# Kernel tuning notes

Hardware: AMD Instinct MI355X
Metric: run time of the kernel (lower is better)

Reference implementation:

```python
import jax, jax.numpy as jnp
import numpy as np

DIM = 512; D_STATE = 8; D_CONV = 3; EXPAND = 1; WIN = 7; N = WIN * WIN
D_INNER = EXPAND * DIM; D_HALF = D_INNER // 2
DT_RANK = -(-DIM // 16)  # 32
E = DT_RANK + 2 * D_STATE  # 48
B_WIN = 512


def _diag_flat(w):
    idx = []
    for s in range(2 * w - 1):
        for r in range(max(0, s - (w - 1)), min(w - 1, s) + 1):
            idx.append(r * w + (s - r))
    return np.array(idx, dtype=np.int32)


def _anti_flat(w):
    idx = []
    for s in range(2 * w - 1):
        for r in range(max(0, s - (w - 1)), min(w - 1, s) + 1):
            c = s - r
            idx.append(r * w + (w - 1 - c))
    return np.array(idx, dtype=np.int32)

DIAG_IDX = jnp.asarray(_diag_flat(WIN))
ANTI_IDX = jnp.asarray(_anti_flat(WIN))
V_IDX = jnp.asarray(np.arange(N).reshape(WIN, WIN).T.reshape(-1).astype(np.int32))


def setup_inputs() -> dict:
    key = jax.random.key(0)
    ks = iter(jax.random.split(key, 32))
    f32 = jnp.float32
    def lin_w(k, out_d, in_d):
        return (jax.random.normal(k, (out_d, in_d), f32) * (in_d ** -0.5)).astype(f32)
    inp = {}
    inp['tokens'] = jax.random.normal(next(ks), (B_WIN, N, DIM), f32)
    for nm in ['pre_h', 'pre_v', 'pre_d', 'pre_a', 'post_h', 'post_v', 'post_d', 'post_a']:
        inp[nm + '_w'] = lin_w(next(ks), DIM, DIM)
        inp[nm + '_b'] = jnp.zeros((DIM,), f32)
    inp['in_proj_w'] = lin_w(next(ks), D_INNER, DIM)
    inp['conv_x_w'] = jax.random.normal(next(ks), (D_HALF, 1, D_CONV), f32) * (D_CONV ** -0.5)
    inp['conv_x_b'] = jnp.zeros((D_HALF,), f32)
    inp['conv_z_w'] = jax.random.normal(next(ks), (D_HALF, 1, D_CONV), f32) * (D_CONV ** -0.5)
    inp['conv_z_b'] = jnp.zeros((D_HALF,), f32)
    inp['x_proj_w'] = lin_w(next(ks), E, D_HALF)
    inp['ln_w'] = jnp.ones((E,), f32)
    inp['ln_b'] = jnp.zeros((E,), f32)
    dt_std = DT_RANK ** -0.5
    inp['dt_proj_w'] = jax.random.uniform(next(ks), (D_HALF, DT_RANK), f32, -dt_std, dt_std)
    u = jax.random.uniform(next(ks), (D_HALF,), f32)
    dt = jnp.clip(jnp.exp(u * (np.log(0.1) - np.log(0.001)) + np.log(0.001)), 1e-4, None)
    inp['dt_proj_b'] = dt + jnp.log(-jnp.expm1(-dt))
    inp['A_log'] = jnp.tile(jnp.log(jnp.arange(1, D_STATE + 1, dtype=f32))[None, :], (D_HALF, 1))
    inp['D_param'] = jnp.ones((D_HALF,), f32)
    inp['out_proj_w'] = lin_w(next(ks), DIM, D_INNER)
    inp['gate_logits'] = jnp.zeros((4,), f32)
    return inp


def _linear(x, W, b=None):
    y = x @ W.T
    return y if b is None else y + b


def _dwconv_same(x, w, b):
    # x: (b, d, l), w: (d, 1, k) depthwise, cross-correlation like torch
    y = jax.lax.conv_general_dilated(x, w, window_strides=(1,), padding='SAME',
                                     dimension_numbers=('NCH', 'OIH', 'NCH'),
                                     feature_group_count=x.shape[1])
    return y + b[None, :, None]


def _layernorm(x, g, b, eps=1e-5):
    m = jnp.mean(x, -1, keepdims=True)
    v = jnp.var(x, -1, keepdims=True)
    return (x - m) * jax.lax.rsqrt(v + eps) * g + b


def _selective_scan(u, delta, A, Bm, Cm, D, delta_bias):
    # u, delta: (b,d,l); A: (d,n); Bm, Cm: (b,n,l); D: (d,)
    delta = jax.nn.softplus(delta + delta_bias[None, :, None])
    u_l = jnp.moveaxis(u, 2, 0)       # (l,b,d)
    d_l = jnp.moveaxis(delta, 2, 0)   # (l,b,d)
    B_l = jnp.moveaxis(Bm, 2, 0)      # (l,b,n)
    C_l = jnp.moveaxis(Cm, 2, 0)      # (l,b,n)
    h0 = jnp.zeros((u.shape[0], u.shape[1], A.shape[1]), u.dtype)  # (b,d,n)

    def step(h, t):
        dt_t, u_t, B_t, C_t = t
        dA = jnp.exp(dt_t[:, :, None] * A[None])          # (b,d,n)
        dBu = dt_t[:, :, None] * B_t[:, None, :] * u_t[:, :, None]
        h = h * dA + dBu
        y = jnp.einsum('bdn,bn->bd', h, C_t)
        return h, y

    _, ys = jax.lax.scan(step, h0, (d_l, u_l, B_l, C_l))
    y = jnp.moveaxis(ys, 0, 2)  # (b,d,l)
    return y + D[None, :, None] * u


def _mamba_core(x_seq, p):
    b, L, _ = x_seq.shape
    xz = _linear(x_seq, p['in_proj_w'])              # (b,l,d_inner)
    xz = jnp.swapaxes(xz, 1, 2)                      # (b,d_inner,l)
    x, z = jnp.split(xz, 2, axis=1)                  # each (b,d_half,l)
    x_conv = jax.nn.silu(_dwconv_same(x, p['conv_x_w'], p['conv_x_b']))
    z_conv = jax.nn.silu(_dwconv_same(z, p['conv_z_w'], p['conv_z_b']))
    A = -jnp.exp(p['A_log'])
    x_dbl = jnp.einsum('bdl,ed->ble', x_conv, p['x_proj_w'])  # (b,l,E)
    x_dbl = _layernorm(x_dbl, p['ln_w'], p['ln_b'])
    dt, Bm, Cm = jnp.split(x_dbl, [DT_RANK, DT_RANK + D_STATE], axis=-1)
    dt = jnp.swapaxes(_linear(dt, p['dt_proj_w']), 1, 2)      # (b,d_half,l)
    Bm = jnp.swapaxes(Bm, 1, 2)                                # (b,n,l)
    Cm = jnp.swapaxes(Cm, 1, 2)
    y = _selective_scan(x_conv, dt, A, Bm, Cm, p['D_param'], p['dt_proj_b'])
    y = jnp.nan_to_num(y)
    y = jnp.concatenate([y, z_conv], axis=1)                   # (b,d_inner,l)
    y = jnp.swapaxes(y, 1, 2)
    return _linear(y, p['out_proj_w'])


def reference(tokens, pre_h_w, pre_h_b, pre_v_w, pre_v_b, pre_d_w, pre_d_b,
              pre_a_w, pre_a_b, in_proj_w, conv_x_w, conv_x_b, conv_z_w, conv_z_b,
              x_proj_w, ln_w, ln_b, dt_proj_w, dt_proj_b, A_log, D_param,
              out_proj_w, post_h_w, post_h_b, post_v_w, post_v_b, post_d_w,
              post_d_b, post_a_w, post_a_b, gate_logits):
    p = dict(in_proj_w=in_proj_w, conv_x_w=conv_x_w, conv_x_b=conv_x_b,
             conv_z_w=conv_z_w, conv_z_b=conv_z_b, x_proj_w=x_proj_w,
             ln_w=ln_w, ln_b=ln_b, dt_proj_w=dt_proj_w, dt_proj_b=dt_proj_b,
             A_log=A_log, D_param=D_param, out_proj_w=out_proj_w)
    rh = _linear(tokens, pre_h_w, pre_h_b)
    rv = _linear(tokens, pre_v_w, pre_v_b)[:, V_IDX, :]
    rd = _linear(tokens, pre_d_w, pre_d_b)[:, DIAG_IDX, :]
    ra = _linear(tokens, pre_a_w, pre_a_b)[:, ANTI_IDX, :]
    r_all = jnp.concatenate([rh, rv, rd, ra], axis=0)
    y_all = _mamba_core(r_all, p)
    yh, yv, yd, ya = jnp.split(y_all, 4, axis=0)
    yh = _linear(yh, post_h_w, post_h_b)
    yv = _linear(yv, post_v_w, post_v_b)
    yd = _linear(yd, post_d_w, post_d_b)
    ya = _linear(ya, post_a_w, post_a_b)
    g = jax.nn.softmax(gate_logits)
    return g[0] * yh + g[1] * yv + g[2] * yd + g[3] * ya
```

## Files before the change

### kernel.cpp

```cpp
#include <hip/hip_runtime.h>
#include <stdint.h>

typedef __attribute__((ext_vector_type(8))) short bf16x8;
typedef __attribute__((ext_vector_type(4))) float f32x4;

__device__ __forceinline__ float bf2f(short u){
  union { float f; uint32_t i; } v; v.i = ((uint32_t)(uint16_t)u) << 16; return v.f;
}
__device__ __forceinline__ short f2bf(float x){
  union { float f; uint32_t i; } v; v.f = x;
  uint32_t r = v.i + 0x7FFFu + ((v.i >> 16) & 1u);
  return (short)(r >> 16);
}

__device__ __forceinline__ void gl_lds16(const short* g, short* l){
  __builtin_amdgcn_global_load_lds(
      (__attribute__((address_space(1))) void*)(short*)g,
      (__attribute__((address_space(3))) void*)l, 16, 0, 0);
}

__device__ const int d_DIAG[49] = {0,1,7,2,8,14,3,9,15,21,4,10,16,22,28,5,11,17,23,29,35,
  6,12,18,24,30,36,42,13,19,25,31,37,43,20,26,32,38,44,27,33,39,45,34,40,46,41,47,48};
__device__ const int d_ANTI[49] = {6,5,13,4,12,20,3,11,19,27,2,10,18,26,34,1,9,17,25,33,41,
  0,8,16,24,32,40,48,7,15,23,31,39,47,14,22,30,38,46,21,29,37,45,28,36,44,35,43,42};

__device__ __forceinline__ int perm_idx(int g, int l){
  if (g == 0) return l;
  if (g == 1) return (l % 7) * 7 + l / 7;
  if (g == 2) return d_DIAG[l];
  return d_ANTI[l];
}

template<int NT>
__device__ __forceinline__ void kcore256(
    const short* aU0, const short* aU1, const short* bU0, const short* bU1,
    short* S, int w, int lane, f32x4 acc[8][4])
{
  int wr = w >> 2, wc = w & 3;
  int mr = lane & 15, quad = lane >> 4;
  int sw = (quad ^ ((mr >> 1) & 3)) * 8;
  auto STAGE = [&](int u, int t){
    short* base = S + (t & 1) * 16384;
    if      (u == 0) gl_lds16(aU0 + t*32, base + (w*32)*32);
    else if (u == 1) gl_lds16(aU1 + t*32, base + (w*32 + 16)*32);
    else if (u == 2) gl_lds16(bU0 + t*32, base + 8192 + (w*32)*32);
    else             gl_lds16(bU1 + t*32, base + 8192 + (w*32 + 16)*32);
  };
  STAGE(0,0); STAGE(1,0); STAGE(2,0); STAGE(3,0);
  if (NT > 1){ STAGE(0,1); STAGE(1,1); }
  asm volatile("s_waitcnt vmcnt(2)" ::: "memory");
  __builtin_amdgcn_s_barrier();
  for (int t = 0; t < NT; ++t){
    const short* Ab = S + (t & 1) * 16384;
    const short* Bb = Ab + 8192;
    bf16x8 bfr[4];
    #pragma unroll
    for (int nf = 0; nf < 4; ++nf)
      bfr[nf] = *(const bf16x8*)(Bb + (wc*64 + nf*16 + mr)*32 + sw);
    #pragma unroll
    for (int ph = 0; ph < 4; ++ph){
      bf16x8 af[2];
      #pragma unroll
      for (int mi = 0; mi < 2; ++mi)
        af[mi] = *(const bf16x8*)(Ab + (wr*128 + (ph*2+mi)*16 + mr)*32 + sw);
      if (ph < 2 && t+1 < NT) STAGE(2+ph, t+1);
      #pragma unroll
      for (int mi = 0; mi < 2; ++mi)
        #pragma unroll
        for (int nf = 0; nf < 4; ++nf)
          acc[ph*2+mi][nf] = __builtin_amdgcn_mfma_f32_16x16x32_bf16(af[mi], bfr[nf], acc[ph*2+mi][nf],0,0,0);
    }
    __builtin_amdgcn_s_barrier();
    if (t+2 < NT){
      STAGE(0, t+2); STAGE(1, t+2);
      asm volatile("s_waitcnt vmcnt(2)" ::: "memory");
    } else if (t+1 < NT){
      asm volatile("s_waitcnt vmcnt(0)" ::: "memory");
    }
    __builtin_amdgcn_s_barrier();
  }
}

template<int NT>
__device__ __forceinline__ void kcore256x128(
    const short* aU0, const short* aU1, const short* bU,
    short* S, int w, int lane, f32x4 acc[4][4])
{
  int wr = w >> 1, wc = w & 1;
  int mr = lane & 15, quad = lane >> 4;
  int sw = (quad ^ ((mr >> 1) & 3)) * 8;
  auto STAGE_A = [&](int t){
    short* base = S + (t & 1) * 12288;
    gl_lds16(aU0 + t*32, base + (w*32)*32);
    gl_lds16(aU1 + t*32, base + (w*32 + 16)*32);
  };
  auto STAGE_B = [&](int t){
    short* base = S + (t & 1) * 12288;
    gl_lds16(bU + t*32, base + 8192 + (w*16)*32);
  };
  STAGE_A(0); STAGE_B(0);
  if (NT > 1) STAGE_A(1);
  asm volatile("s_waitcnt vmcnt(2)" ::: "memory");
  __builtin_amdgcn_s_barrier();
  for (int t = 0; t < NT; ++t){
    const short* Ab = S + (t & 1) * 12288;
    const short* Bb = Ab + 8192;
    bf16x8 bfr[4];
    #pragma unroll
    for (int nf = 0; nf < 4; ++nf)
      bfr[nf] = *(const bf16x8*)(Bb + (wc*64 + nf*16 + mr)*32 + sw);
    #pragma unroll
    for (int ph = 0; ph < 4; ++ph){
      bf16x8 af = *(const bf16x8*)(Ab + (wr*64 + ph*16 + mr)*32 + sw);
      if (ph == 1 && t+1 < NT) STAGE_B(t+1);
      #pragma unroll
      for (int nf = 0; nf < 4; ++nf)
        acc[ph][nf] = __builtin_amdgcn_mfma_f32_16x16x32_bf16(af, bfr[nf], acc[ph][nf],0,0,0);
    }
    __builtin_amdgcn_s_barrier();
    if (t+2 < NT){
      STAGE_A(t+2);
      asm volatile("s_waitcnt vmcnt(2)" ::: "memory");
    } else if (t+1 < NT){
      asm volatile("s_waitcnt vmcnt(0)" ::: "memory");
    }
    __builtin_amdgcn_s_barrier();
  }
}

__global__ __launch_bounds__(256) void k_conv_all(
    const float* __restrict__ in_proj,
    const float* __restrict__ pw0, const float* __restrict__ pw1,
    const float* __restrict__ pw2, const float* __restrict__ pw3,
    const float* __restrict__ xpw, const float* __restrict__ dtw,
    short* __restrict__ inp_bf, short* __restrict__ postw_bf,
    short* __restrict__ xpw_bf, short* __restrict__ dtw_bf)
{
  int q = blockIdx.x*256 + threadIdx.x;
  const float* src; short* dst; int off;
  if (q < 65536){ src = in_proj; dst = inp_bf; off = q; }
  else if (q < 65536 + 262144){
    int r = q - 65536; int g = r >> 16; int loc = r & 65535;
    src = (g==0)?pw0:(g==1)?pw1:(g==2)?pw2:pw3;
    dst = postw_bf + g*262144; off = loc;
  }
  else if (q < 65536 + 262144 + 3072){ src = xpw; dst = xpw_bf; off = q - (65536+262144); }
  else { src = dtw; dst = dtw_bf; off = q - (65536+262144+3072); }
  float4 v = *(const float4*)(src + off*4);
  uint32_t p0 = (uint32_t)(uint16_t)f2bf(v.x) | ((uint32_t)(uint16_t)f2bf(v.y) << 16);
  uint32_t p1 = (uint32_t)(uint16_t)f2bf(v.z) | ((uint32_t)(uint16_t)f2bf(v.w) << 16);
  uint2 p; p.x = p0; p.y = p1;
  *(uint2*)(dst + off*4) = p;
}

__global__ __launch_bounds__(256) void k_transp(
    const float* __restrict__ pw0, const float* __restrict__ pw1,
    const float* __restrict__ pw2, const float* __restrict__ pw3,
    const float* __restrict__ outp,
    short* __restrict__ wpreT, short* __restrict__ woutT)
{
  __shared__ float tile[64][65];
  int which = blockIdx.y;
  const float* src = (which==0)?pw0:(which==1)?pw1:(which==2)?pw2:(which==3)?pw3:outp;
  short* dst = (which < 4) ? (wpreT + which*262144) : woutT;
  int bi = blockIdx.x >> 3, bj = blockIdx.x & 7;
  int r0 = bi*64, c0 = bj*64;
  int t = threadIdx.x;
  int row = t >> 2, cg = t & 3;
  const float4* s4 = (const float4*)(src + (r0+row)*512 + c0 + cg*16);
  #pragma unroll
  for (int i=0;i<4;i++){
    float4 v = s4[i];
    tile[row][cg*16 + i*4 + 0] = v.x;
    tile[row][cg*16 + i*4 + 1] = v.y;
    tile[row][cg*16 + i*4 + 2] = v.z;
    tile[row][cg*16 + i*4 + 3] = v.w;
  }
  __syncthreads();
  int oc = t >> 2;
  short tmp[16];
  #pragma unroll
  for (int i=0;i<16;i++) tmp[i] = f2bf(tile[cg*16 + i][oc]);
  short* dp = dst + (size_t)(c0+oc)*512 + r0 + cg*16;
  *(bf16x8*)(dp)     = *(bf16x8*)tmp;
  *(bf16x8*)(dp + 8) = *((bf16x8*)tmp + 1);
}

__global__ __launch_bounds__(256) void k_tok(const float* __restrict__ t, short* __restrict__ o){
  int i = (blockIdx.x*256 + threadIdx.x) * 4;
  float4 v = *(const float4*)(t + i);
  uint32_t p0 = (uint32_t)(uint16_t)f2bf(v.x) | ((uint32_t)(uint16_t)f2bf(v.y) << 16);
  uint32_t p1 = (uint32_t)(uint16_t)f2bf(v.z) | ((uint32_t)(uint16_t)f2bf(v.w) << 16);
  uint2 p; p.x = p0; p.y = p1;
  *(uint2*)(o + i) = p;
}

__global__ __launch_bounds__(256) void k_bxz_gains(const float* __restrict__ in_proj,
    const float* __restrict__ b0, const float* __restrict__ b1,
    const float* __restrict__ b2, const float* __restrict__ b3,
    const float* __restrict__ gl,
    const float* __restrict__ pb0, const float* __restrict__ pb1,
    const float* __restrict__ pb2, const float* __restrict__ pb3,
    float* __restrict__ bxz, float* __restrict__ gains, float* __restrict__ biasc)
{
  if (blockIdx.x < 8){
    int idx = blockIdx.x*256 + threadIdx.x;
    int g = idx >> 9, i = idx & 511;
    const float* bb = (g==0)?b0:(g==1)?b1:(g==2)?b2:b3;
    float s = 0.f;
    for (int t=0;t<512;t++) s += in_proj[i*512+t]*bb[t];
    bxz[idx] = s;
  } else {
    float m = fmaxf(fmaxf(gl[0], gl[1]), fmaxf(gl[2], gl[3]));
    float e0 = expf(gl[0]-m), e1 = expf(gl[1]-m), e2 = expf(gl[2]-m), e3 = expf(gl[3]-m);
    float s = e0+e1+e2+e3;
    float g0 = e0/s, g1 = e1/s, g2 = e2/s, g3 = e3/s;
    int t = threadIdx.x;
    if (t == 0){ gains[0]=g0; gains[1]=g1; gains[2]=g2; gains[3]=g3; }
    biasc[t]     = g0*pb0[t]     + g1*pb1[t]     + g2*pb2[t]     + g3*pb3[t];
    biasc[t+256] = g0*pb0[t+256] + g1*pb1[t+256] + g2*pb2[t+256] + g3*pb3[t+256];
  }
}

__device__ __forceinline__ void mfma_2x4_k(const short* a0, const short* a1,
    const short* b0, const short* b1, const short* b2, const short* b3,
    int K, f32x4 acc[2][4])
{
  for (int k0 = 0; k0 < K; k0 += 32){
    bf16x8 av0 = *(const bf16x8*)(a0 + k0);
    bf16x8 av1 = *(const bf16x8*)(a1 + k0);
    bf16x8 bv0 = *(const bf16x8*)(b0 + k0);
    bf16x8 bv1 = *(const bf16x8*)(b1 + k0);
    bf16x8 bv2 = *(const bf16x8*)(b2 + k0);
    bf16x8 bv3 = *(const bf16x8*)(b3 + k0);
    acc[0][0] = __builtin_amdgcn_mfma_f32_16x16x32_bf16(av0, bv0, acc[0][0],0,0,0);
    acc[0][1] = __builtin_amdgcn_mfma_f32_16x16x32_bf16(av0, bv1, acc[0][1],0,0,0);
    acc[0][2] = __builtin_amdgcn_mfma_f32_16x16x32_bf16(av0, bv2, acc[0][2],0,0,0);
    acc[0][3] = __builtin_amdgcn_mfma_f32_16x16x32_bf16(av0, bv3, acc[0][3],0,0,0);
    acc[1][0] = __builtin_amdgcn_mfma_f32_16x16x32_bf16(av1, bv0, acc[1][0],0,0,0);
    acc[1][1] = __builtin_amdgcn_mfma_f32_16x16x32_bf16(av1, bv1, acc[1][1],0,0,0);
    acc[1][2] = __builtin_amdgcn_mfma_f32_16x16x32_bf16(av1, bv2, acc[1][2],0,0,0);
    acc[1][3] = __builtin_amdgcn_mfma_f32_16x16x32_bf16(av1, bv3, acc[1][3],0,0,0);
  }
}

__global__ __launch_bounds__(256) void k_wfuse(const short* __restrict__ inp_bf,
    const short* __restrict__ wpreT, const short* __restrict__ postw_bf,
    const short* __restrict__ woutT, const float* __restrict__ gains,
    short* __restrict__ wxz, short* __restrict__ wogc)
{
  int z = blockIdx.z; int g = z & 3, which = z >> 2;
  int bn = blockIdx.x * 64, bm = blockIdx.y * 128;
  int lane = threadIdx.x & 63, wave = threadIdx.x >> 6;
  int mr = lane & 15, qk = (lane >> 4) * 8, quad = lane >> 4;
  const short* Am = which ? (postw_bf + g*262144) : inp_bf;
  const short* Bm = which ? woutT : (wpreT + g*262144);
  const short* a0 = Am + (bm + wave*32 + mr)*512 + qk;
  const short* a1 = a0 + 16*512;
  const short* b0 = Bm + (bn +  0 + mr)*512 + qk;
  const short* b1 = Bm + (bn + 16 + mr)*512 + qk;
  const short* b2 = Bm + (bn + 32 + mr)*512 + qk;
  const short* b3 = Bm + (bn + 48 + mr)*512 + qk;
  f32x4 acc[2][4] = {};
  mfma_2x4_k(a0, a1, b0, b1, b2, b3, 512, acc);
  float gain = which ? gains[g] : 1.f;
  #pragma unroll
  for (int s=0;s<2;s++)
    #pragma unroll
    for (int t=0;t<4;t++)
      #pragma unroll
      for (int r=0;r<4;r++){
        int row = bm + wave*32 + s*16 + quad*4 + r;
        int col = bn + t*16 + mr;
        if (which) wogc[row*2048 + g*512 + col] = f2bf(gain * acc[s][t][r]);
        else       wxz[g*262144 + row*512 + col] = f2bf(acc[s][t][r]);
      }
}

__global__ __launch_bounds__(512) void k_gemm1(const short* __restrict__ tok,
    const short* __restrict__ wxz, const float* __restrict__ bxz, short* __restrict__ xz)
{
  __shared__ __align__(16) short S[24576];
  int bid = blockIdx.x;
  int swz = (bid & 7) * 196 + (bid >> 3);
  int g = swz / 392, rem = swz - g*392;
  int bm = (rem >> 2) * 256, bn = (rem & 3) * 128;
  int tid = threadIdx.x, lane = tid & 63, w = tid >> 6;

  int rl = lane >> 2;
  int gch = ((lane & 3) ^ ((lane >> 3) & 3)) * 8;
  const short* aU[2];
  #pragma unroll
  for (int j = 0; j < 2; ++j){
    int grow = bm + w*32 + j*16 + rl;
    int b = grow / 49, l49 = grow - b*49;
    int sl = perm_idx(g, l49);
    aU[j] = tok + ((size_t)(b*49 + sl))*512 + gch;
  }
  const short* bU = wxz + (size_t)g*262144 + (size_t)(bn + w*16 + rl)*512 + gch;

  f32x4 acc[4][4] = {};
  kcore256x128<16>(aU[0], aU[1], bU, S, w, lane, acc);

  int wr = w >> 1, wc = w & 1, mr = lane & 15, quad = lane >> 4;
  #pragma unroll
  for (int mf = 0; mf < 4; ++mf)
    #pragma unroll
    for (int rr = 0; rr < 4; ++rr){
      int row = bm + wr*64 + mf*16 + quad*4 + rr;
      int b = row / 49, l = row - b*49;
      size_t orow = ((size_t)(g*512 + b)*49 + l)*512;
      #pragma unroll
      for (int nf = 0; nf < 4; ++nf){
        int col = bn + wc*64 + nf*16 + mr;
        xz[orow + col] = f2bf(acc[mf][nf][rr] + bxz[g*512 + col]);
      }
    }
}

__global__ __launch_bounds__(256) void k_conv(const short* __restrict__ xz,
    const float* __restrict__ cxw, const float* __restrict__ cxb,
    const float* __restrict__ czw, const float* __restrict__ czb,
    short* __restrict__ ycat)
{
  int t = threadIdx.x;
  int oct = t & 63, lstart = t >> 6;
  int ch0 = oct * 8;
  bool isx = ch0 < 256;
  int cc0 = isx ? ch0 : ch0 - 256;
  const float* wsrc = isx ? cxw : czw;
  const float* bsrc = isx ? cxb : czb;
  float w0[8], w1[8], w2[8], bb[8];
  #pragma unroll
  for (int e=0;e<8;e++){
    w0[e] = wsrc[(cc0+e)*3]; w1[e] = wsrc[(cc0+e)*3+1]; w2[e] = wsrc[(cc0+e)*3+2];
    bb[e] = bsrc[cc0+e];
  }
  int gb = blockIdx.x; int g = gb >> 9, b = gb & 511;
  const short* src = xz + (size_t)gb*25088 + ch0;
  short* dst = ycat + (size_t)(b*49)*2048 + g*512 + ch0;
  for (int l = lstart; l < 49; l += 4){
    bf16x8 vm = {}, vp = {};
    bf16x8 v0 = *(const bf16x8*)(src + l*512);
    if (l > 0)  vm = *(const bf16x8*)(src + (l-1)*512);
    if (l < 48) vp = *(const bf16x8*)(src + (l+1)*512);
    short ov[8];
    #pragma unroll
    for (int e=0;e<8;e++){
      float x = w0[e]*bf2f(vm[e]) + w1[e]*bf2f(v0[e]) + w2[e]*bf2f(vp[e]) + bb[e];
      ov[e] = f2bf(x / (1.f + __expf(-x)));
    }
    *(bf16x8*)(dst + l*2048) = *(bf16x8*)ov;
  }
}

__global__ __launch_bounds__(256) void k_xproj(const short* __restrict__ ycat,
    const short* __restrict__ xpw_bf, const float* __restrict__ lnw, const float* __restrict__ lnb,
    const short* __restrict__ dtw_bf, const float* __restrict__ dtb,
    short* __restrict__ dtln, float* __restrict__ bc)
{
  __shared__ __align__(16) char smem[36864];
  float* xd = (float*)smem;
  short* xln = (short*)(smem + 26624);

  int bm = blockIdx.x * 128;
  int g = bm / 25088;
  int tid = threadIdx.x, lane = tid & 63, w = tid >> 6;
  int mr = lane & 15, quad = lane >> 4, qk = quad * 8;

  {
    const short* ap[2];
    #pragma unroll
    for (int s=0;s<2;s++)
      ap[s] = ycat + (size_t)(bm - g*25088 + w*32 + s*16 + mr)*2048 + g*512 + qk;
    f32x4 acc[2][3] = {};
    #pragma unroll
    for (int k0 = 0; k0 < 256; k0 += 32){
      bf16x8 av[2];
      #pragma unroll
      for (int s=0;s<2;s++) av[s] = *(const bf16x8*)(ap[s] + k0);
      #pragma unroll
      for (int t=0;t<3;t++){
        bf16x8 bv = *(const bf16x8*)(xpw_bf + (t*16 + mr)*256 + qk + k0);
        #pragma unroll
        for (int s=0;s<2;s++)
          acc[s][t] = __builtin_amdgcn_mfma_f32_16x16x32_bf16(av[s], bv, acc[s][t],0,0,0);
      }
    }
    #pragma unroll
    for (int s=0;s<2;s++)
      #pragma unroll
      for (int t=0;t<3;t++)
        #pragma unroll
        for (int r=0;r<4;r++)
          xd[(w*32 + s*16 + quad*4 + r)*52 + t*16 + mr] = acc[s][t][r];
  }
  __syncthreads();

  if (tid < 128){
    f32x4* xr4 = (f32x4*)(xd + tid*52);
    f32x4 s = xr4[0];
    #pragma unroll
    for (int i=1;i<12;i++) s += xr4[i];
    float m = (s[0]+s[1]+s[2]+s[3]) * (1.f/48.f);
    f32x4 vs = {};
    #pragma unroll
    for (int i=0;i<12;i++){ f32x4 d = xr4[i] - m; vs += d*d; }
    float var = (vs[0]+vs[1]+vs[2]+vs[3]) * (1.f/48.f);
    float rstd = rsqrtf(var + 1e-5f);
    const f32x4* g4 = (const f32x4*)lnw;
    const f32x4* b4 = (const f32x4*)lnb;
    uint32_t* xlr = (uint32_t*)(xln + tid*40);
    #pragma unroll
    for (int i=0;i<8;i++){
      f32x4 v = (xr4[i] - m) * rstd * g4[i] + b4[i];
      xlr[2*i]   = (uint32_t)(uint16_t)f2bf(v[0]) | ((uint32_t)(uint16_t)f2bf(v[1]) << 16);
      xlr[2*i+1] = (uint32_t)(uint16_t)f2bf(v[2]) | ((uint32_t)(uint16_t)f2bf(v[3]) << 16);
    }
    f32x4* bco = (f32x4*)(bc + (size_t)(bm + tid)*16);
    #pragma unroll
    for (int i=8;i<12;i++)
      bco[i-8] = (xr4[i] - m) * rstd * g4[i] + b4[i];
  }
  __syncthreads();

  {
    bf16x8 a[2];
    #pragma unroll
    for (int s=0;s<2;s++)
      a[s] = *(const bf16x8*)(xln + (w*32 + s*16 + mr)*40 + qk);
    #pragma unroll 4
    for (int nt=0; nt<16; nt++){
      int col = nt*16 + mr;
      bf16x8 bv = *(const bf16x8*)(dtw_bf + col*32 + qk);
      float dtbv = dtb[col];
      #pragma unroll
      for (int s=0;s<2;s++){
        f32x4 acc = {};
        acc = __builtin_amdgcn_mfma_f32_16x16x32_bf16(a[s], bv, acc,0,0,0);
        #pragma unroll
        for (int r=0;r<4;r++){
          int grow = bm + w*32 + s*16 + quad*4 + r;
          float dtv = acc[r] + dtbv;
          float e  = __expf(dtv);
          float sp = __logf(1.f + e);
          float delta = (dtv > 15.f) ? dtv : sp;
          dtln[(size_t)grow*256 + col] = f2bf(delta);
        }
      }
    }
  }
}

__global__ __launch_bounds__(256) void k_scan(short* __restrict__ ycat,
    const short* __restrict__ dtln, const float* __restrict__ bc,
    const float* __restrict__ Alog, const float* __restrict__ Dp)
{
  __shared__ __align__(16) float bcs[784];
  int gb = blockIdx.x; int g = gb >> 9, b = gb & 511;
  int d = threadIdx.x;
  if (d < 196) ((f32x4*)bcs)[d] = ((const f32x4*)(bc + (size_t)gb*784))[d];
  __syncthreads();

  float A[8], h[8];
  {
    f32x4 a0 = *(const f32x4*)(Alog + d*8);
    f32x4 a1 = *(const f32x4*)(Alog + d*8 + 4);
    #pragma unroll
    for (int n=0;n<4;n++){ A[n] = -__expf(a0[n]); A[n+4] = -__expf(a1[n]); h[n]=0.f; h[n+4]=0.f; }
  }
  float Dpar = Dp[d];

  const short* dptr = dtln + (size_t)gb*49*256 + d;
  short* uptr = ycat + (size_t)(b*49)*2048 + g*512 + d;

  float dn = bf2f(dptr[0]);
  float un = bf2f(uptr[0]);
  for (int l=0;l<49;l++){
    float delta = dn, u = un;
    if (l < 48){ dn = bf2f(dptr[(l+1)*256]); un = bf2f(uptr[(l+1)*2048]); }
    const f32x4* bcr = (const f32x4*)(bcs + l*16);
    f32x4 B0 = bcr[0], B1 = bcr[1], C0 = bcr[2], C1 = bcr[3];
    float du = delta * u;
    float y = 0.f;
    #pragma unroll
    for (int n=0;n<4;n++){
      h[n] = h[n]*__expf(delta*A[n]) + du*B0[n];
      y += h[n]*C0[n];
    }
    #pragma unroll
    for (int n=0;n<4;n++){
      h[n+4] = h[n+4]*__expf(delta*A[n+4]) + du*B1[n];
      y += h[n+4]*C1[n];
    }
    uptr[l*2048] = f2bf(y + Dpar*u);
  }
}

__global__ __launch_bounds__(512) void k_gemmF(const short* __restrict__ ycat,
    const short* __restrict__ wogc, const float* __restrict__ biasc,
    float* __restrict__ out)
{
  __shared__ __align__(16) short S[32768];
  int bid = blockIdx.x;
  int bm = (bid >> 1) * 256, bn = (bid & 1) * 256;
  int tid = threadIdx.x, lane = tid & 63, w = tid >> 6;

  int rl = lane >> 2;
  int gch = ((lane & 3) ^ ((lane >> 3) & 3)) * 8;
  const short* aU0 = ycat + (size_t)(bm + w*32      + rl)*2048 + gch;
  const short* aU1 = ycat + (size_t)(bm + w*32 + 16 + rl)*2048 + gch;
  const short* bU0 = wogc + (size_t)(bn + w*32      + rl)*2048 + gch;
  const short* bU1 = wogc + (size_t)(bn + w*32 + 16 + rl)*2048 + gch;

  f32x4 acc[8][4] = {};
  kcore256<64>(aU0, aU1, bU0, bU1, S, w, lane, acc);

  int wr = w >> 2, wc = w & 3, mr = lane & 15, quad = lane >> 4;
  #pragma unroll
  for (int mf = 0; mf < 8; ++mf)
    #pragma unroll
    for (int rr = 0; rr < 4; ++rr){
      int row = bm + wr*128 + mf*16 + quad*4 + rr;
      float* orow = out + (size_t)row*512;
      #pragma unroll
      for (int nf = 0; nf < 4; ++nf){
        int col = bn + wc*64 + nf*16 + mr;
        orow[col] = acc[mf][nf][rr] + biasc[col];
      }
    }
}

extern "C" void kernel_launch(void* const* d_in, const int* in_sizes, int n_in,
                              void* d_out, int out_size, void* d_ws, size_t ws_size,
                              hipStream_t stream)
{
  const float* tokens    = (const float*)d_in[0];
  const float* pre_w[4]  = {(const float*)d_in[1], (const float*)d_in[3], (const float*)d_in[5], (const float*)d_in[7]};
  const float* pre_b[4]  = {(const float*)d_in[2], (const float*)d_in[4], (const float*)d_in[6], (const float*)d_in[8]};
  const float* post_w[4] = {(const float*)d_in[9], (const float*)d_in[11], (const float*)d_in[13], (const float*)d_in[15]};
  const float* post_b[4] = {(const float*)d_in[10], (const float*)d_in[12], (const float*)d_in[14], (const float*)d_in[16]};
  const float* in_proj   = (const float*)d_in[17];
  const float* conv_x_w  = (const float*)d_in[18];
  const float* conv_x_b  = (const float*)d_in[19];
  const float* conv_z_w  = (const float*)d_in[20];
  const float* conv_z_b  = (const float*)d_in[21];
  const float* x_proj_w  = (const float*)d_in[22];
  const float* ln_w      = (const float*)d_in[23];
  const float* ln_b      = (const float*)d_in[24];
  const float* dt_proj_w = (const float*)d_in[25];
  const float* dt_proj_b = (const float*)d_in[26];
  const float* A_log     = (const float*)d_in[27];
  const float* D_param   = (const float*)d_in[28];
  const float* out_proj  = (const float*)d_in[29];
  const float* gate_log  = (const float*)d_in[30];

  char* ws = (char*)d_ws;
  size_t o = 0;
  short* tok_bf   = (short*)(ws + o); o += 25690112;
  short* wpreT    = (short*)(ws + o); o += 2097152;
  short* inp_bf   = (short*)(ws + o); o += 524288;
  short* postw_bf = (short*)(ws + o); o += 2097152;
  short* woutT    = (short*)(ws + o); o += 524288;
  short* wogc     = (short*)(ws + o); o += 2097152;
  short* wxz      = (short*)(ws + o); o += 2097152;
  short* xpw_bf   = (short*)(ws + o); o += 24576;
  short* dtw_bf   = (short*)(ws + o); o += 16384;
  float* bxz      = (float*)(ws + o); o += 8192;
  float* gains    = (float*)(ws + o); o += 64;
  float* biasc    = (float*)(ws + o); o += 2048;
  size_t xz_off = o;
  short* xz       = (short*)(ws + o); o += 102760448;
  short* ycat     = (short*)(ws + o); o += 102760448;
  short* dtln     = (short*)(ws + xz_off);
  float* bc       = (float*)(ws + xz_off + 51380224);

  k_conv_all<<<1300, 256, 0, stream>>>(in_proj,
      post_w[0], post_w[1], post_w[2], post_w[3],
      x_proj_w, dt_proj_w, inp_bf, postw_bf, xpw_bf, dtw_bf);
  k_transp<<<dim3(64,5), 256, 0, stream>>>(pre_w[0], pre_w[1], pre_w[2], pre_w[3],
      out_proj, wpreT, woutT);
  k_tok<<<12544, 256, 0, stream>>>(tokens, tok_bf);
  k_bxz_gains<<<9, 256, 0, stream>>>(in_proj, pre_b[0], pre_b[1], pre_b[2], pre_b[3],
      gate_log, post_b[0], post_b[1], post_b[2], post_b[3], bxz, gains, biasc);
  k_wfuse<<<dim3(8,4,8), 256, 0, stream>>>(inp_bf, wpreT, postw_bf, woutT, gains, wxz, wogc);
  k_gemm1<<<dim3(1568), 512, 0, stream>>>(tok_bf, wxz, bxz, xz);
  k_conv<<<2048, 256, 0, stream>>>(xz, conv_x_w, conv_x_b, conv_z_w, conv_z_b, ycat);
  k_xproj<<<784, 256, 0, stream>>>(ycat, xpw_bf, ln_w, ln_b, dtw_bf, dt_proj_b, dtln, bc);
  k_scan<<<2048, 256, 0, stream>>>(ycat, dtln, bc, A_log, D_param);
  k_gemmF<<<dim3(196), 512, 0, stream>>>(ycat, wogc, biasc, (float*)d_out);
}
```

Before: 482.9 us.

## Fuse depthwise conv+SiLU into input GEMM epilogue and retile final GEMM

```diff
diff --git a/kernel.cpp b/kernel.cpp
--- a/kernel.cpp
+++ b/kernel.cpp
@@ -29,56 +29,6 @@
   if (g == 1) return (l % 7) * 7 + l / 7;
   if (g == 2) return d_DIAG[l];
   return d_ANTI[l];
-}
-
-template<int NT>
-__device__ __forceinline__ void kcore256(
-    const short* aU0, const short* aU1, const short* bU0, const short* bU1,
-    short* S, int w, int lane, f32x4 acc[8][4])
-{
-  int wr = w >> 2, wc = w & 3;
-  int mr = lane & 15, quad = lane >> 4;
-  int sw = (quad ^ ((mr >> 1) & 3)) * 8;
-  auto STAGE = [&](int u, int t){
-    short* base = S + (t & 1) * 16384;
-    if      (u == 0) gl_lds16(aU0 + t*32, base + (w*32)*32);
-    else if (u == 1) gl_lds16(aU1 + t*32, base + (w*32 + 16)*32);
-    else if (u == 2) gl_lds16(bU0 + t*32, base + 8192 + (w*32)*32);
-    else             gl_lds16(bU1 + t*32, base + 8192 + (w*32 + 16)*32);
-  };
-  STAGE(0,0); STAGE(1,0); STAGE(2,0); STAGE(3,0);
-  if (NT > 1){ STAGE(0,1); STAGE(1,1); }
-  asm volatile("s_waitcnt vmcnt(2)" ::: "memory");
-  __builtin_amdgcn_s_barrier();
-  for (int t = 0; t < NT; ++t){
-    const short* Ab = S + (t & 1) * 16384;
-    const short* Bb = Ab + 8192;
-    bf16x8 bfr[4];
-    #pragma unroll
-    for (int nf = 0; nf < 4; ++nf)
-      bfr[nf] = *(const bf16x8*)(Bb + (wc*64 + nf*16 + mr)*32 + sw);
-    #pragma unroll
-    for (int ph = 0; ph < 4; ++ph){
-      bf16x8 af[2];
-      #pragma unroll
-      for (int mi = 0; mi < 2; ++mi)
-        af[mi] = *(const bf16x8*)(Ab + (wr*128 + (ph*2+mi)*16 + mr)*32 + sw);
-      if (ph < 2 && t+1 < NT) STAGE(2+ph, t+1);
-      #pragma unroll
-      for (int mi = 0; mi < 2; ++mi)
-        #pragma unroll
-        for (int nf = 0; nf < 4; ++nf)
-          acc[ph*2+mi][nf] = __builtin_amdgcn_mfma_f32_16x16x32_bf16(af[mi], bfr[nf], acc[ph*2+mi][nf],0,0,0);
-    }
-    __builtin_amdgcn_s_barrier();
-    if (t+2 < NT){
-      STAGE(0, t+2); STAGE(1, t+2);
-      asm volatile("s_waitcnt vmcnt(2)" ::: "memory");
-    } else if (t+1 < NT){
-      asm volatile("s_waitcnt vmcnt(0)" ::: "memory");
-    }
-    __builtin_amdgcn_s_barrier();
-  }
 }
 
 template<int NT>
@@ -277,14 +227,19 @@
       }
 }
 
-__global__ __launch_bounds__(512) void k_gemm1(const short* __restrict__ tok,
-    const short* __restrict__ wxz, const float* __restrict__ bxz, short* __restrict__ xz)
+__global__ __launch_bounds__(512) void k_gemm1c(const short* __restrict__ tok,
+    const short* __restrict__ wxz, const float* __restrict__ bxz,
+    const float* __restrict__ cxw, const float* __restrict__ cxb,
+    const float* __restrict__ czw, const float* __restrict__ czb,
+    short* __restrict__ ycat)
 {
   __shared__ __align__(16) short S[24576];
   int bid = blockIdx.x;
-  int swz = (bid & 7) * 196 + (bid >> 3);
-  int g = swz / 392, rem = swz - g*392;
-  int bm = (rem >> 2) * 256, bn = (rem & 3) * 128;
+  int swz = (bid & 7) * 206 + (bid >> 3);
+  int g = swz / 412, rem = swz - g*412;
+  int blk = rem >> 2, bn = (rem & 3) * 128;
+  int bm = blk * 245;
+  int nreal = min(245, 25088 - bm);
   int tid = threadIdx.x, lane = tid & 63, w = tid >> 6;
 
   int rl = lane >> 2;
@@ -292,8 +247,11 @@
   const short* aU[2];
   #pragma unroll
   for (int j = 0; j < 2; ++j){
-    int grow = bm + w*32 + j*16 + rl;
-    int b = grow / 49, l49 = grow - b*49;
+    int p = w*32 + j*16 + rl;
+    int pr = (p < nreal) ? p : (nreal - 1);
+    int q49 = pr / 49;
+    int l49 = pr - q49*49;
+    int b = blk*5 + q49;
     int sl = perm_idx(g, l49);
     aU[j] = tok + ((size_t)(b*49 + sl))*512 + gch;
   }
@@ -303,54 +261,51 @@
   kcore256x128<16>(aU[0], aU[1], bU, S, w, lane, acc);
 
   int wr = w >> 1, wc = w & 1, mr = lane & 15, quad = lane >> 4;
+  int rowgrp = tid >> 3, oct = tid & 7;
   #pragma unroll
-  for (int mf = 0; mf < 4; ++mf)
-    #pragma unroll
-    for (int rr = 0; rr < 4; ++rr){
-      int row = bm + wr*64 + mf*16 + quad*4 + rr;
-      int b = row / 49, l = row - b*49;
-      size_t orow = ((size_t)(g*512 + b)*49 + l)*512;
-      #pragma unroll
-      for (int nf = 0; nf < 4; ++nf){
-        int col = bn + wc*64 + nf*16 + mr;
-        xz[orow + col] = f2bf(acc[mf][nf][rr] + bxz[g*512 + col]);
+  for (int h = 0; h < 2; ++h){
+    if (wc == h){
+      #pragma unroll
+      for (int mf = 0; mf < 4; ++mf)
+        #pragma unroll
+        for (int nf = 0; nf < 4; ++nf)
+          #pragma unroll
+          for (int rr = 0; rr < 4; ++rr){
+            int row = wr*64 + mf*16 + quad*4 + rr;
+            int col = nf*16 + mr;
+            S[row*72 + col] = f2bf(acc[mf][nf][rr] + bxz[g*512 + bn + h*64 + col]);
+          }
+    }
+    __syncthreads();
+    int colbase = bn + h*64 + oct*8;
+    bool isx = colbase < 256;
+    const float* wsrc = isx ? cxw : czw;
+    const float* bsrc = isx ? cxb : czb;
+    int cc0 = isx ? colbase : colbase - 256;
+    float w0[8], w1[8], w2[8], cb[8];
+    #pragma unroll
+    for (int e = 0; e < 8; ++e){
+      w0[e] = wsrc[(cc0+e)*3]; w1[e] = wsrc[(cc0+e)*3+1]; w2[e] = wsrc[(cc0+e)*3+2];
+      cb[e] = bsrc[cc0+e];
+    }
+    for (int i = 0; i < 4; ++i){
+      int p = rowgrp + 64*i;
+      if (p < nreal){
+        int l = p - (p/49)*49;
+        bf16x8 vm = {}, vp = {};
+        bf16x8 v0 = *(const bf16x8*)(S + p*72 + oct*8);
+        if (l > 0)  vm = *(const bf16x8*)(S + (p-1)*72 + oct*8);
+        if (l < 48) vp = *(const bf16x8*)(S + (p+1)*72 + oct*8);
+        short ov[8];
+        #pragma unroll
+        for (int e = 0; e < 8; ++e){
+          float x = w0[e]*bf2f(vm[e]) + w1[e]*bf2f(v0[e]) + w2[e]*bf2f(vp[e]) + cb[e];
+          ov[e] = f2bf(x / (1.f + __expf(-x)));
+        }
+        *(bf16x8*)(ycat + (size_t)(bm + p)*2048 + g*512 + colbase) = *(bf16x8*)ov;
       }
     }
-}
-
-__global__ __launch_bounds__(256) void k_conv(const short* __restrict__ xz,
-    const float* __restrict__ cxw, const float* __restrict__ cxb,
-    const float* __restrict__ czw, const float* __restrict__ czb,
-    short* __restrict__ ycat)
-{
-  int t = threadIdx.x;
-  int oct = t & 63, lstart = t >> 6;
-  int ch0 = oct * 8;
-  bool isx = ch0 < 256;
-  int cc0 = isx ? ch0 : ch0 - 256;
-  const float* wsrc = isx ? cxw : czw;
-  const float* bsrc = isx ? cxb : czb;
-  float w0[8], w1[8], w2[8], bb[8];
-  #pragma unroll
-  for (int e=0;e<8;e++){
-    w0[e] = wsrc[(cc0+e)*3]; w1[e] = wsrc[(cc0+e)*3+1]; w2[e] = wsrc[(cc0+e)*3+2];
-    bb[e] = bsrc[cc0+e];
-  }
-  int gb = blockIdx.x; int g = gb >> 9, b = gb & 511;
-  const short* src = xz + (size_t)gb*25088 + ch0;
-  short* dst = ycat + (size_t)(b*49)*2048 + g*512 + ch0;
-  for (int l = lstart; l < 49; l += 4){
-    bf16x8 vm = {}, vp = {};
-    bf16x8 v0 = *(const bf16x8*)(src + l*512);
-    if (l > 0)  vm = *(const bf16x8*)(src + (l-1)*512);
-    if (l < 48) vp = *(const bf16x8*)(src + (l+1)*512);
-    short ov[8];
-    #pragma unroll
-    for (int e=0;e<8;e++){
-      float x = w0[e]*bf2f(vm[e]) + w1[e]*bf2f(v0[e]) + w2[e]*bf2f(vp[e]) + bb[e];
-      ov[e] = f2bf(x / (1.f + __expf(-x)));
-    }
-    *(bf16x8*)(dst + l*2048) = *(bf16x8*)ov;
+    __syncthreads();
   }
 }
 
@@ -501,27 +456,27 @@
     const short* __restrict__ wogc, const float* __restrict__ biasc,
     float* __restrict__ out)
 {
-  __shared__ __align__(16) short S[32768];
+  __shared__ __align__(16) short S[24576];
   int bid = blockIdx.x;
-  int bm = (bid >> 1) * 256, bn = (bid & 1) * 256;
+  int swz = (bid & 7) * 49 + (bid >> 3);
+  int bm = (swz >> 2) * 256, bn = (swz & 3) * 128;
   int tid = threadIdx.x, lane = tid & 63, w = tid >> 6;
 
   int rl = lane >> 2;
   int gch = ((lane & 3) ^ ((lane >> 3) & 3)) * 8;
   const short* aU0 = ycat + (size_t)(bm + w*32      + rl)*2048 + gch;
   const short* aU1 = ycat + (size_t)(bm + w*32 + 16 + rl)*2048 + gch;
-  const short* bU0 = wogc + (size_t)(bn + w*32      + rl)*2048 + gch;
-  const short* bU1 = wogc + (size_t)(bn + w*32 + 16 + rl)*2048 + gch;
-
-  f32x4 acc[8][4] = {};
-  kcore256<64>(aU0, aU1, bU0, bU1, S, w, lane, acc);
-
-  int wr = w >> 2, wc = w & 3, mr = lane & 15, quad = lane >> 4;
+  const short* bU  = wogc + (size_t)(bn + w*16      + rl)*2048 + gch;
+
+  f32x4 acc[4][4] = {};
+  kcore256x128<64>(aU0, aU1, bU, S, w, lane, acc);
+
+  int wr = w >> 1, wc = w & 1, mr = lane & 15, quad = lane >> 4;
   #pragma unroll
-  for (int mf = 0; mf < 8; ++mf)
+  for (int mf = 0; mf < 4; ++mf)
     #pragma unroll
     for (int rr = 0; rr < 4; ++rr){
-      int row = bm + wr*128 + mf*16 + quad*4 + rr;
+      int row = bm + wr*64 + mf*16 + quad*4 + rr;
       float* orow = out + (size_t)row*512;
       #pragma unroll
       for (int nf = 0; nf < 4; ++nf){
@@ -569,11 +524,11 @@
   float* bxz      = (float*)(ws + o); o += 8192;
   float* gains    = (float*)(ws + o); o += 64;
   float* biasc    = (float*)(ws + o); o += 2048;
-  size_t xz_off = o;
-  short* xz       = (short*)(ws + o); o += 102760448;
+  size_t scratch_off = o;
+  o += 102760448;
   short* ycat     = (short*)(ws + o); o += 102760448;
-  short* dtln     = (short*)(ws + xz_off);
-  float* bc       = (float*)(ws + xz_off + 51380224);
+  short* dtln     = (short*)(ws + scratch_off);
+  float* bc       = (float*)(ws + scratch_off + 51380224);
 
   k_conv_all<<<1300, 256, 0, stream>>>(in_proj,
       post_w[0], post_w[1], post_w[2], post_w[3],
@@ -584,9 +539,9 @@
   k_bxz_gains<<<9, 256, 0, stream>>>(in_proj, pre_b[0], pre_b[1], pre_b[2], pre_b[3],
       gate_log, post_b[0], post_b[1], post_b[2], post_b[3], bxz, gains, biasc);
   k_wfuse<<<dim3(8,4,8), 256, 0, stream>>>(inp_bf, wpreT, postw_bf, woutT, gains, wxz, wogc);
-  k_gemm1<<<dim3(1568), 512, 0, stream>>>(tok_bf, wxz, bxz, xz);
-  k_conv<<<2048, 256, 0, stream>>>(xz, conv_x_w, conv_x_b, conv_z_w, conv_z_b, ycat);
+  k_gemm1c<<<dim3(1648), 512, 0, stream>>>(tok_bf, wxz, bxz,
+      conv_x_w, conv_x_b, conv_z_w, conv_z_b, ycat);
   k_xproj<<<784, 256, 0, stream>>>(ycat, xpw_bf, ln_w, ln_b, dtw_bf, dt_proj_b, dtln, bc);
   k_scan<<<2048, 256, 0, stream>>>(ycat, dtln, bc, A_log, D_param);
-  k_gemmF<<<dim3(196), 512, 0, stream>>>(ycat, wogc, biasc, (float*)d_out);
-}
+  k_gemmF<<<dim3(392), 512, 0, stream>>>(ycat, wogc, biasc, (float*)d_out);
+}
```

Result: faster. 453.1 us (-6.2%).
